# Performance work log

Measured on AMD Instinct MI355X. Metric: run time of the kernel, lower is better.

Reference implementation:

```python
import jax, jax.numpy as jnp
import numpy as np

N = 100000
E = 1600000
IN_CH = 64
HID = 32
HEADS = 4
OUT_CH = 32
NEG_SLOPE = 0.2  # PyG GATConv default


def setup_inputs() -> dict:
    key = jax.random.key(0)
    ks = jax.random.split(key, 10)
    x = jax.random.normal(ks[0], (N, IN_CH), dtype=jnp.float32)
    edge_index = jax.random.randint(ks[1], (2, E), 0, N, dtype=jnp.int64)
    s = 0.1
    W1 = jax.random.normal(ks[2], (IN_CH, HEADS * HID), dtype=jnp.float32) * s
    att_src1 = jax.random.normal(ks[3], (HEADS, HID), dtype=jnp.float32) * s
    att_dst1 = jax.random.normal(ks[4], (HEADS, HID), dtype=jnp.float32) * s
    b1 = jnp.zeros((HEADS * HID,), dtype=jnp.float32)
    W2 = jax.random.normal(ks[5], (HEADS * HID, OUT_CH), dtype=jnp.float32) * s
    att_src2 = jax.random.normal(ks[6], (1, OUT_CH), dtype=jnp.float32) * s
    att_dst2 = jax.random.normal(ks[7], (1, OUT_CH), dtype=jnp.float32) * s
    b2 = jnp.zeros((OUT_CH,), dtype=jnp.float32)
    return {"x": x, "edge_index": edge_index, "W1": W1, "att_src1": att_src1,
            "att_dst1": att_dst1, "b1": b1, "W2": W2, "att_src2": att_src2,
            "att_dst2": att_dst2, "b2": b2}


def gat_conv(x, src, dst, W, a_src, a_dst, b, heads, out_ch):
    # Linear transform: [N, H, C]
    h = (x @ W).reshape(N, heads, out_ch)
    # Per-node attention logits: [N, H]
    al_src = jnp.sum(h * a_src[None], axis=-1)
    al_dst = jnp.sum(h * a_dst[None], axis=-1)
    # Per-edge attention (gather): [E', H]
    e = jax.nn.leaky_relu(al_src[src] + al_dst[dst], negative_slope=NEG_SLOPE)
    # Segment softmax over incoming edges of each dst node
    m = jax.ops.segment_max(e, dst, num_segments=N)
    ex = jnp.exp(e - m[dst])
    denom = jax.ops.segment_sum(ex, dst, num_segments=N)
    alpha = ex / denom[dst]
    # Weighted messages + scatter-add: [N, H, C]
    msg = h[src] * alpha[:, :, None]
    out = jax.ops.segment_sum(msg, dst, num_segments=N)
    return out.reshape(N, heads * out_ch) + b


def reference(x, edge_index, W1, att_src1, att_dst1, b1, W2, att_src2, att_dst2, b2):
    # PyG GATConv adds self-loops by default
    loops = jnp.arange(N, dtype=edge_index.dtype)
    src = jnp.concatenate([edge_index[0], loops])
    dst = jnp.concatenate([edge_index[1], loops])
    h = gat_conv(x, src, dst, W1, att_src1, att_dst1, b1, HEADS, HID)
    h = jax.nn.elu(h)
    out = gat_conv(h, src, dst, W2, att_src2, att_dst2, b2, 1, OUT_CH)
    return out
```

## Files before the change

### kernel.cpp

```cpp
#include <hip/hip_runtime.h>
#include <hip/hip_bf16.h>

typedef __hip_bfloat16 bf16;
typedef short bf16x8 __attribute__((ext_vector_type(8)));
typedef float f32x4 __attribute__((ext_vector_type(4)));

#define IN_CH 64
#define HID 32
#define HEADS 4
#define C1 128
#define OUTC 32
#define NEGSLOPE 0.2f

#define NSEG 196
#define SEGSH 9
#define BINCAP 9216
#define P1CHUNK 4096

__device__ __forceinline__ float lrelu(float v) { return v > 0.f ? v : NEGSLOPE * v; }
__device__ __forceinline__ float elu(float v) { return v > 0.f ? v : __expf(v) - 1.f; }
__device__ __forceinline__ float lo16f(unsigned u) { return __uint_as_float(u << 16); }
__device__ __forceinline__ float hi16f(unsigned u) { return __uint_as_float(u & 0xFFFF0000u); }
__device__ __forceinline__ short f2bs(float f) {
  bf16 b = __float2bfloat16(f);
  return *reinterpret_cast<short*>(&b);
}
__device__ __forceinline__ unsigned pack2(float lo, float hi) {
  unsigned short l = (unsigned short)f2bs(lo);
  unsigned short h = (unsigned short)f2bs(hi);
  return ((unsigned)h << 16) | (unsigned)l;
}
__device__ __forceinline__ void mac8(float* acc, float wv, uint4 qq) {
  acc[0] += wv * lo16f(qq.x); acc[1] += wv * hi16f(qq.x);
  acc[2] += wv * lo16f(qq.y); acc[3] += wv * hi16f(qq.y);
  acc[4] += wv * lo16f(qq.z); acc[5] += wv * hi16f(qq.z);
  acc[6] += wv * lo16f(qq.w); acc[7] += wv * hi16f(qq.w);
}



__global__ __launch_bounds__(256) void k_p1_k1(
    const int* __restrict__ ew, int* __restrict__ cursor, unsigned* __restrict__ tmp,
    int E, int nN,
    const float* __restrict__ x, const float* __restrict__ W1,
    const float* __restrict__ attS, const float* __restrict__ attD,
    bf16* __restrict__ hB, float* __restrict__ alS, float* __restrict__ alD) {
  if (blockIdx.x < 391) {
    __shared__ unsigned stageE[P1CHUNK];
    __shared__ unsigned char stageB[P1CHUNK];
    __shared__ int cnt1[256];
    __shared__ int excl1[NSEG];
    __shared__ int pos1[NSEG];
    __shared__ int gb[NSEG];
    int t = threadIdx.x;
    int chunk0 = blockIdx.x * P1CHUNK;
    int cntE = min(P1CHUNK, E - chunk0);
    unsigned myE[16];
    int myB[16];
    cnt1[t] = 0;
    __syncthreads();
    #pragma unroll
    for (int i = 0; i < 16; ++i) {
      int j = t + i * 256;
      if (j < cntE) {
        int e = chunk0 + j;
        int s = ew[e];
        int d = ew[E + e];
        int b = d >> SEGSH;
        myE[i] = ((unsigned)(d & 511) << 17) | (unsigned)s;
        myB[i] = b;
        atomicAdd(&cnt1[b], 1);
      } else {
        myB[i] = -1;
      }
    }
    __syncthreads();
    int v = cnt1[t];
    #pragma unroll
    for (int off = 1; off < 256; off <<= 1) {
      int tv = (t >= off) ? cnt1[t - off] : 0;
      __syncthreads();
      cnt1[t] += tv;
      __syncthreads();
    }
    int ex = cnt1[t] - v;
    if (t < NSEG) {
      excl1[t] = ex;
      pos1[t] = ex;
      gb[t] = (v > 0) ? atomicAdd(&cursor[t], v) : 0;
    }
    __syncthreads();
    #pragma unroll
    for (int i = 0; i < 16; ++i) {
      if (myB[i] >= 0) {
        int r = atomicAdd(&pos1[myB[i]], 1);
        stageE[r] = myE[i];
        stageB[r] = (unsigned char)myB[i];
      }
    }
    __syncthreads();
    for (int j = t; j < cntE; j += 256) {
      int b = stageB[j];
      int idx = gb[b] + (j - excl1[b]);
      if (idx < BINCAP) tmp[b * BINCAP + idx] = stageE[j];
    }
    return;
  }
  int lane = threadIdx.x & 63;
  int m = lane & 15;
  int q = lane >> 4;
  int wid = ((blockIdx.x - 391) * 256 + threadIdx.x) >> 6;
  int nW = 512 * 4;
  bf16x8 wf[8][2];
  #pragma unroll
  for (int ct = 0; ct < 8; ++ct)
    #pragma unroll
    for (int ks = 0; ks < 2; ++ks)
      #pragma unroll
      for (int j = 0; j < 8; ++j)
        wf[ct][ks][j] = f2bs(W1[(ks * 32 + q * 8 + j) * C1 + ct * 16 + m]);
  float aS[8], aD[8];
  #pragma unroll
  for (int ct = 0; ct < 8; ++ct) {
    int g = ct >> 1;
    int cc = (ct & 1) * 16 + m;
    aS[ct] = attS[g * HID + cc];
    aD[ct] = attD[g * HID + cc];
  }
  int nT = nN >> 4;
  for (int nt = wid; nt < nT; nt += nW) {
    int n0 = nt * 16;
    const float* xr = x + (size_t)(n0 + m) * IN_CH;
    bf16x8 af[2];
    #pragma unroll
    for (int ks = 0; ks < 2; ++ks) {
      float4 v0 = *(const float4*)(xr + ks * 32 + q * 8);
      float4 v1 = *(const float4*)(xr + ks * 32 + q * 8 + 4);
      af[ks][0] = f2bs(v0.x); af[ks][1] = f2bs(v0.y);
      af[ks][2] = f2bs(v0.z); af[ks][3] = f2bs(v0.w);
      af[ks][4] = f2bs(v1.x); af[ks][5] = f2bs(v1.y);
      af[ks][6] = f2bs(v1.z); af[ks][7] = f2bs(v1.w);
    }
    f32x4 acc[8];
    #pragma unroll
    for (int ct = 0; ct < 8; ++ct) acc[ct] = (f32x4){0.f, 0.f, 0.f, 0.f};
    #pragma unroll
    for (int ct = 0; ct < 8; ++ct) {
      acc[ct] = __builtin_amdgcn_mfma_f32_16x16x32_bf16(af[0], wf[ct][0], acc[ct], 0, 0, 0);
      acc[ct] = __builtin_amdgcn_mfma_f32_16x16x32_bf16(af[1], wf[ct][1], acc[ct], 0, 0, 0);
    }
    float pS[4][4], pD[4][4];
    #pragma unroll
    for (int g = 0; g < 4; ++g)
      #pragma unroll
      for (int r = 0; r < 4; ++r) { pS[g][r] = 0.f; pD[g][r] = 0.f; }
    #pragma unroll
    for (int ct = 0; ct < 8; ++ct) {
      int g = ct >> 1;
      #pragma unroll
      for (int r = 0; r < 4; ++r) {
        float v = acc[ct][r];
        hB[(size_t)(n0 + q * 4 + r) * C1 + ct * 16 + m] = __float2bfloat16(v);
        pS[g][r] += v * aS[ct];
        pD[g][r] += v * aD[ct];
      }
    }
    #pragma unroll
    for (int off = 1; off < 16; off <<= 1) {
      #pragma unroll
      for (int g = 0; g < 4; ++g)
        #pragma unroll
        for (int r = 0; r < 4; ++r) {
          pS[g][r] += __shfl_xor(pS[g][r], off);
          pD[g][r] += __shfl_xor(pD[g][r], off);
        }
    }
    if (m == 0) {
      #pragma unroll
      for (int r = 0; r < 4; ++r) {
        int n = n0 + q * 4 + r;
        #pragma unroll
        for (int g = 0; g < 4; ++g) {
          alS[(size_t)n * 4 + g] = pS[g][r];
          alD[(size_t)n * 4 + g] = pD[g][r];
        }
      }
    }
  }
}

__global__ __launch_bounds__(512) void k_p2(
    const unsigned* __restrict__ tmp, const int* __restrict__ cursor,
    int* __restrict__ csr, int2* __restrict__ rsdg, int nN) {
  __shared__ int cnt2[512];
  __shared__ int pos2[512];
  __shared__ unsigned ldsE[BINCAP];
  int b = blockIdx.x;
  int t = threadIdx.x;
  int count = min(cursor[b], BINCAP);
  const unsigned* bin = tmp + b * BINCAP;
  cnt2[t] = 0;
  __syncthreads();
  for (int j = t; j < count; j += 512) {
    int d = bin[j] >> 17;
    atomicAdd(&cnt2[d], 1);
  }
  __syncthreads();
  int v = cnt2[t];
  #pragma unroll
  for (int off = 1; off < 512; off <<= 1) {
    int tv = (t >= off) ? cnt2[t - off] : 0;
    __syncthreads();
    cnt2[t] += tv;
    __syncthreads();
  }
  int ex = cnt2[t] - v;
  pos2[t] = ex;
  __syncthreads();
  for (int j = t; j < count; j += 512) {
    unsigned e = bin[j];
    int d = e >> 17;
    int r = atomicAdd(&pos2[d], 1);
    ldsE[r] = e & 0x1FFFFu;
  }
  __syncthreads();
  for (int j = t; j < count; j += 512)
    csr[b * BINCAP + j] = (int)ldsE[j];
  int n = (b << SEGSH) + t;
  if (n < nN) rsdg[n] = make_int2(b * BINCAP + ex, v);
}

__global__ __launch_bounds__(256) void k2(
    const unsigned* __restrict__ hb, const float* __restrict__ alS, const float* __restrict__ alD,
    const int2* __restrict__ rsdg, const int* __restrict__ csr,
    const float* __restrict__ b1, const float* __restrict__ W2,
    const float* __restrict__ attS2, const float* __restrict__ attD2,
    bf16* __restrict__ h2B, float* __restrict__ alS2, float* __restrict__ alD2, int nN) {
  __shared__ float w2s[C1 * OUTC];
  for (int i = threadIdx.x; i < C1 * OUTC; i += 256) {
    int k = i >> 5;
    int ch = i & 31;
    int ch4 = ch >> 2;
    int cl = ch & 3;
    int sw = k >> 5;
    w2s[(k << 5) + (((ch4 ^ sw) << 2) | cl)] = W2[i];
  }
  __syncthreads();
  int t = blockIdx.x * 256 + threadIdx.x;
  int n = t >> 4;
  int g = t & 3;
  int qt = (t >> 2) & 3;
  int2 rd = rsdg[n];
  int rs = rd.x;
  int re = rd.x + rd.y;
  float ad = alD[(size_t)n * HEADS + g];
  float acc[HID];
  #pragma unroll
  for (int c = 0; c < HID; ++c) acc[c] = 0.f;
  float denom = 0.f;
  if (qt == 0) {
    float wv = __expf(lrelu(alS[(size_t)n * HEADS + g] + ad));
    denom += wv;
    const uint4* hr = (const uint4*)(hb + (size_t)n * 64 + g * 16);
    uint4 q0 = hr[0], q1 = hr[1], q2 = hr[2], q3 = hr[3];
    mac8(acc + 0, wv, q0); mac8(acc + 8, wv, q1);
    mac8(acc + 16, wv, q2); mac8(acc + 24, wv, q3);
  }
  for (int i = rs + qt; i < re; i += 4) {
    int s = csr[i];
    float a = alS[(size_t)s * 4 + g];
    const uint4* hr = (const uint4*)(hb + (size_t)s * 64 + g * 16);
    uint4 q0 = hr[0], q1 = hr[1], q2 = hr[2], q3 = hr[3];
    float wv = __expf(lrelu(a + ad));
    denom += wv;
    mac8(acc + 0, wv, q0); mac8(acc + 8, wv, q1);
    mac8(acc + 16, wv, q2); mac8(acc + 24, wv, q3);
  }
  denom += __shfl_xor(denom, 4);
  denom += __shfl_xor(denom, 8);
  #pragma unroll
  for (int c = 0; c < HID; ++c) {
    acc[c] += __shfl_xor(acc[c], 4);
    acc[c] += __shfl_xor(acc[c], 8);
  }
  float inv = 1.f / denom;
  #pragma unroll
  for (int c = 0; c < HID; ++c)
    acc[c] = elu(acc[c] * inv + b1[g * HID + c]);
  float partial[8];
  #pragma unroll
  for (int j = 0; j < 8; ++j) partial[j] = 0.f;
  #pragma unroll
  for (int kk = 0; kk < HID; ++kk) {
    float v = acc[kk];
    int base = (g * HID + kk) << 5;
    float4 w0 = *(const float4*)&w2s[base + (((qt * 2 + 0) ^ g) << 2)];
    float4 w1 = *(const float4*)&w2s[base + (((qt * 2 + 1) ^ g) << 2)];
    partial[0] += v * w0.x; partial[1] += v * w0.y;
    partial[2] += v * w0.z; partial[3] += v * w0.w;
    partial[4] += v * w1.x; partial[5] += v * w1.y;
    partial[6] += v * w1.z; partial[7] += v * w1.w;
  }
  #pragma unroll
  for (int j = 0; j < 8; ++j) {
    partial[j] += __shfl_xor(partial[j], 1);
    partial[j] += __shfl_xor(partial[j], 2);
  }
  float a2s[8], a2d[8];
  {
    const float4* sv = (const float4*)(attS2 + qt * 8);
    *(float4*)&a2s[0] = sv[0]; *(float4*)&a2s[4] = sv[1];
    const float4* dv = (const float4*)(attD2 + qt * 8);
    *(float4*)&a2d[0] = dv[0]; *(float4*)&a2d[4] = dv[1];
  }
  float ps = 0.f, pd = 0.f;
  #pragma unroll
  for (int j = 0; j < 8; ++j) {
    ps += partial[j] * a2s[j];
    pd += partial[j] * a2d[j];
  }
  ps += __shfl_xor(ps, 4); ps += __shfl_xor(ps, 8);
  pd += __shfl_xor(pd, 4); pd += __shfl_xor(pd, 8);
  if ((t & 15) == 0) {
    alS2[n] = ps;
    alD2[n] = pd;
  }
  if (g == 0) {
    uint4 uu;
    uu.x = pack2(partial[0], partial[1]);
    uu.y = pack2(partial[2], partial[3]);
    uu.z = pack2(partial[4], partial[5]);
    uu.w = pack2(partial[6], partial[7]);
    *reinterpret_cast<uint4*>(h2B + (size_t)n * OUTC + qt * 8) = uu;
  }
}

__global__ __launch_bounds__(256) void k4(
    const unsigned* __restrict__ h2b, const float* __restrict__ alS2,
    const float* __restrict__ alD2, const int2* __restrict__ rsdg, const int* __restrict__ csr,
    const float* __restrict__ b2, float* __restrict__ out, int nN) {
  int t = blockIdx.x * 256 + threadIdx.x;
  int n = t >> 4;
  int l16 = t & 15;
  int c4 = l16 & 3;
  int qt = l16 >> 2;
  int2 rd = rsdg[n];
  int rs = rd.x;
  int re = rd.x + rd.y;
  float ad = alD2[n];
  float acc[8];
  #pragma unroll
  for (int c = 0; c < 8; ++c) acc[c] = 0.f;
  float denom = 0.f;
  if (qt == 0) {
    float wv = __expf(lrelu(alS2[n] + ad));
    denom += wv;
    uint4 qq = *(const uint4*)(h2b + (size_t)n * 16 + c4 * 4);
    mac8(acc, wv, qq);
  }
  for (int i = rs + qt; i < re; i += 4) {
    int s = csr[i];
    float a = alS2[s];
    uint4 qq = *(const uint4*)(h2b + (size_t)s * 16 + c4 * 4);
    float wv = __expf(lrelu(a + ad));
    denom += wv;
    mac8(acc, wv, qq);
  }
  denom += __shfl_xor(denom, 4);
  denom += __shfl_xor(denom, 8);
  #pragma unroll
  for (int c = 0; c < 8; ++c) {
    acc[c] += __shfl_xor(acc[c], 4);
    acc[c] += __shfl_xor(acc[c], 8);
  }
  if (qt == 0) {
    float inv = 1.f / denom;
    float4 ba = *(const float4*)(b2 + c4 * 8);
    float4 bb = *(const float4*)(b2 + c4 * 8 + 4);
    float4 o0, o1;
    o0.x = acc[0] * inv + ba.x;
    o0.y = acc[1] * inv + ba.y;
    o0.z = acc[2] * inv + ba.z;
    o0.w = acc[3] * inv + ba.w;
    o1.x = acc[4] * inv + bb.x;
    o1.y = acc[5] * inv + bb.y;
    o1.z = acc[6] * inv + bb.z;
    o1.w = acc[7] * inv + bb.w;
    *(float4*)(out + (size_t)n * OUTC + c4 * 8) = o0;
    *(float4*)(out + (size_t)n * OUTC + c4 * 8 + 4) = o1;
  }
}


extern "C" void kernel_launch(void* const* d_in, const int* in_sizes, int n_in,
                              void* d_out, int out_size, void* d_ws, size_t ws_size,
                              hipStream_t stream) {
  {
    const int expect[10] = {6400000, 3200000, 8192, 128, 128, 128, 4096, 32, 32, 32};
    bool ok = (n_in == 10) && (out_size == 3200000);
    for (int i = 0; i < 10 && ok; ++i) ok = (in_sizes[i] == expect[i]);
    if (!ok) { *(volatile int*)0 = 1; }
  }

  const float* x     = (const float*)d_in[0];
  const int*   ew    = (const int*)d_in[1];
  const float* W1    = (const float*)d_in[2];
  const float* attS1 = (const float*)d_in[3];
  const float* attD1 = (const float*)d_in[4];
  const float* b1    = (const float*)d_in[5];
  const float* W2    = (const float*)d_in[6];
  const float* attS2 = (const float*)d_in[7];
  const float* attD2 = (const float*)d_in[8];
  const float* b2    = (const float*)d_in[9];
  float* out = (float*)d_out;

  const int nN = in_sizes[0] / IN_CH;
  const int E  = in_sizes[1] / 2;

  auto ALN = [](size_t v) { return (v + 255) & ~(size_t)255; };
  char* p = (char*)d_ws;
  bf16*  hB   = (bf16*)p;  p += ALN((size_t)nN * C1 * 2);
  float* alS1v= (float*)p; p += ALN((size_t)nN * 4 * 4);
  float* alD1v= (float*)p; p += ALN((size_t)nN * 4 * 4);
  bf16*  h2B  = (bf16*)p;  p += ALN((size_t)nN * OUTC * 2);
  float* alS2v= (float*)p; p += ALN((size_t)nN * 4);
  float* alD2v= (float*)p; p += ALN((size_t)nN * 4);
  int* cursor = (int*)p;   p += ALN((size_t)NSEG * 4);
  unsigned* tmp = (unsigned*)p; p += ALN((size_t)NSEG * BINCAP * 4);
  int* csr    = (int*)p;   p += ALN((size_t)NSEG * BINCAP * 4);
  int2* rsdg  = (int2*)p;  p += ALN((size_t)nN * 8);
  if ((size_t)(p - (char*)d_ws) > ws_size) { *(volatile int*)0 = 2; }

  hipMemsetAsync(cursor, 0, (size_t)NSEG * 4, stream);
  k_p1_k1<<<391 + 512, 256, 0, stream>>>(ew, cursor, tmp, E, nN,
                                         x, W1, attS1, attD1, hB, alS1v, alD1v);
  k_p2<<<NSEG, 512, 0, stream>>>(tmp, cursor, csr, rsdg, nN);
  k2<<<(nN * 16) / 256, 256, 0, stream>>>((const unsigned*)hB, alS1v, alD1v,
                                          rsdg, csr, b1, W2, attS2, attD2,
                                          h2B, alS2v, alD2v, nN);
  k4<<<(nN * 16) / 256, 256, 0, stream>>>((const unsigned*)h2B, alS2v, alD2v,
                                          rsdg, csr, b2, out, nN);
}
```

Baseline: 260.2 us.

## Sort nodes by in-degree into a permutation to balance gather kernels

```diff
diff --git a/kernel.cpp b/kernel.cpp
--- a/kernel.cpp
+++ b/kernel.cpp
@@ -16,6 +16,7 @@
 #define SEGSH 9
 #define BINCAP 9216
 #define P1CHUNK 4096
+#define DBINS 64
 
 __device__ __forceinline__ float lrelu(float v) { return v > 0.f ? v : NEGSLOPE * v; }
 __device__ __forceinline__ float elu(float v) { return v > 0.f ? v : __expf(v) - 1.f; }
@@ -191,15 +192,17 @@
 
 __global__ __launch_bounds__(512) void k_p2(
     const unsigned* __restrict__ tmp, const int* __restrict__ cursor,
-    int* __restrict__ csr, int2* __restrict__ rsdg, int nN) {
+    int* __restrict__ csr, int2* __restrict__ rsdg, int* __restrict__ ghist, int nN) {
   __shared__ int cnt2[512];
   __shared__ int pos2[512];
+  __shared__ int dh[DBINS];
   __shared__ unsigned ldsE[BINCAP];
   int b = blockIdx.x;
   int t = threadIdx.x;
   int count = min(cursor[b], BINCAP);
   const unsigned* bin = tmp + b * BINCAP;
   cnt2[t] = 0;
+  if (t < DBINS) dh[t] = 0;
   __syncthreads();
   for (int j = t; j < count; j += 512) {
     int d = bin[j] >> 17;
@@ -227,12 +230,55 @@
   for (int j = t; j < count; j += 512)
     csr[b * BINCAP + j] = (int)ldsE[j];
   int n = (b << SEGSH) + t;
-  if (n < nN) rsdg[n] = make_int2(b * BINCAP + ex, v);
+  if (n < nN) {
+    rsdg[n] = make_int2(b * BINCAP + ex, v);
+    atomicAdd(&dh[min(v, DBINS - 1)], 1);
+  }
+  __syncthreads();
+  if (t < DBINS && dh[t] > 0) atomicAdd(&ghist[t], dh[t]);
+}
+
+__global__ void k_scan64(const int* __restrict__ ghist, int* __restrict__ gcur) {
+  __shared__ int sm[DBINS];
+  int t = threadIdx.x;
+  int v = ghist[t];
+  sm[t] = v;
+  __syncthreads();
+  #pragma unroll
+  for (int off = 1; off < DBINS; off <<= 1) {
+    int tv = (t >= off) ? sm[t - off] : 0;
+    __syncthreads();
+    sm[t] += tv;
+    __syncthreads();
+  }
+  gcur[t] = sm[t] - v;
+}
+
+__global__ __launch_bounds__(256) void k_p3(
+    const int2* __restrict__ rsdg, int* __restrict__ gcur,
+    int* __restrict__ perm, int nN) {
+  __shared__ int h[DBINS], base[DBINS], rk[DBINS];
+  int t = threadIdx.x;
+  int n = blockIdx.x * 256 + t;
+  if (t < DBINS) { h[t] = 0; rk[t] = 0; }
+  __syncthreads();
+  int b = -1;
+  if (n < nN) {
+    b = min(rsdg[n].y, DBINS - 1);
+    atomicAdd(&h[b], 1);
+  }
+  __syncthreads();
+  if (t < DBINS && h[t] > 0) base[t] = atomicAdd(&gcur[t], h[t]);
+  __syncthreads();
+  if (n < nN) {
+    int r = atomicAdd(&rk[b], 1);
+    perm[base[b] + r] = n;
+  }
 }
 
 __global__ __launch_bounds__(256) void k2(
     const unsigned* __restrict__ hb, const float* __restrict__ alS, const float* __restrict__ alD,
-    const int2* __restrict__ rsdg, const int* __restrict__ csr,
+    const int2* __restrict__ rsdg, const int* __restrict__ csr, const int* __restrict__ perm,
     const float* __restrict__ b1, const float* __restrict__ W2,
     const float* __restrict__ attS2, const float* __restrict__ attD2,
     bf16* __restrict__ h2B, float* __restrict__ alS2, float* __restrict__ alD2, int nN) {
@@ -247,7 +293,7 @@
   }
   __syncthreads();
   int t = blockIdx.x * 256 + threadIdx.x;
-  int n = t >> 4;
+  int n = perm[t >> 4];
   int g = t & 3;
   int qt = (t >> 2) & 3;
   int2 rd = rsdg[n];
@@ -338,9 +384,10 @@
 __global__ __launch_bounds__(256) void k4(
     const unsigned* __restrict__ h2b, const float* __restrict__ alS2,
     const float* __restrict__ alD2, const int2* __restrict__ rsdg, const int* __restrict__ csr,
+    const int* __restrict__ perm,
     const float* __restrict__ b2, float* __restrict__ out, int nN) {
   int t = blockIdx.x * 256 + threadIdx.x;
-  int n = t >> 4;
+  int n = perm[t >> 4];
   int l16 = t & 15;
   int c4 = l16 & 3;
   int qt = l16 >> 2;
@@ -426,18 +473,23 @@
   float* alS2v= (float*)p; p += ALN((size_t)nN * 4);
   float* alD2v= (float*)p; p += ALN((size_t)nN * 4);
   int* cursor = (int*)p;   p += ALN((size_t)NSEG * 4);
+  int* ghist  = (int*)p;   p += ALN((size_t)DBINS * 4);
+  int* gcur   = (int*)p;   p += ALN((size_t)DBINS * 4);
+  int* perm   = (int*)p;   p += ALN((size_t)nN * 4);
   unsigned* tmp = (unsigned*)p; p += ALN((size_t)NSEG * BINCAP * 4);
   int* csr    = (int*)p;   p += ALN((size_t)NSEG * BINCAP * 4);
   int2* rsdg  = (int2*)p;  p += ALN((size_t)nN * 8);
   if ((size_t)(p - (char*)d_ws) > ws_size) { *(volatile int*)0 = 2; }
 
-  hipMemsetAsync(cursor, 0, (size_t)NSEG * 4, stream);
+  hipMemsetAsync(cursor, 0, (size_t)((char*)gcur - (char*)cursor), stream);
   k_p1_k1<<<391 + 512, 256, 0, stream>>>(ew, cursor, tmp, E, nN,
                                          x, W1, attS1, attD1, hB, alS1v, alD1v);
-  k_p2<<<NSEG, 512, 0, stream>>>(tmp, cursor, csr, rsdg, nN);
+  k_p2<<<NSEG, 512, 0, stream>>>(tmp, cursor, csr, rsdg, ghist, nN);
+  k_scan64<<<1, DBINS, 0, stream>>>(ghist, gcur);
+  k_p3<<<(nN + 255) / 256, 256, 0, stream>>>(rsdg, gcur, perm, nN);
   k2<<<(nN * 16) / 256, 256, 0, stream>>>((const unsigned*)hB, alS1v, alD1v,
-                                          rsdg, csr, b1, W2, attS2, attD2,
+                                          rsdg, csr, perm, b1, W2, attS2, attD2,
                                           h2B, alS2v, alD2v, nN);
   k4<<<(nN * 16) / 256, 256, 0, stream>>>((const unsigned*)h2B, alS2v, alD2v,
-                                          rsdg, csr, b2, out, nN);
-}
+                                          rsdg, csr, perm, b2, out, nN);
+}
```

After: 268.8 us. 3.3% more time.
